# Optimization experiments

Measured on AMD Instinct MI355X. Metric: run time of the kernel, lower is better.

## Reference

```python
import jax, jax.numpy as jnp
import numpy as np

V, E, L, H, B, T = 32000, 1024, 6, 16, 4, 1024
HS = E // H
FF = 4 * E


def setup_inputs() -> dict:
    key = jax.random.key(0)
    ks = jax.random.split(key, 16)
    s = 0.02
    n = lambda k, shp: jax.random.normal(k, shp, jnp.float32) * s
    return {
        "tokens": jax.random.randint(ks[0], (B, T), 0, V),
        "tok_emb": n(ks[1], (V, E)),
        "pos_emb": n(ks[2], (T, E)),
        "Wq": n(ks[3], (L, E, E)),
        "Wk": n(ks[4], (L, E, E)),
        "Wv": n(ks[5], (L, E, E)),
        "Wo": n(ks[6], (L, E, E)),
        "ln1_g": jnp.ones((L, E), jnp.float32),
        "ln1_b": jnp.zeros((L, E), jnp.float32),
        "W1": n(ks[7], (L, E, FF)),
        "b1": jnp.zeros((L, FF), jnp.float32),
        "W2": n(ks[8], (L, FF, E)),
        "b2": jnp.zeros((L, E), jnp.float32),
        "ln2_g": jnp.ones((L, E), jnp.float32),
        "ln2_b": jnp.zeros((L, E), jnp.float32),
        "lmh_w": n(ks[9], (E, V)),
        "lmh_b": jnp.zeros((V,), jnp.float32),
    }


def _layernorm(x, g, b):
    m = jnp.mean(x, axis=-1, keepdims=True)
    v = jnp.var(x, axis=-1, keepdims=True)
    return (x - m) * jax.lax.rsqrt(v + 1e-5) * g + b


def _forward(tokens, tok_emb, pos_emb, Wq, Wk, Wv, Wo, ln1_g, ln1_b,
             W1, b1, W2, b2, ln2_g, ln2_b, lmh_w, lmh_b):
    Bb, Tt = tokens.shape
    x = tok_emb[tokens] + pos_emb[:Tt]  # [B,T,E]
    mask = jnp.tril(jnp.ones((Tt, Tt), bool))  # causal
    scale = jnp.float32(E) ** -0.5  # NOTE: original scales by emb_dim, not head_size

    def block(x, p):
        wq, wk, wv, wo, g1, be1, w1, bb1, w2, bb2, g2, be2 = p
        h = _layernorm(x, g1, be1)
        q = (h @ wq).reshape(Bb, Tt, H, HS)
        k = (h @ wk).reshape(Bb, Tt, H, HS)
        v = (h @ wv).reshape(Bb, Tt, H, HS)
        scores = jnp.einsum('bqhd,bkhd->bhqk', q, k) * scale
        scores = jnp.where(mask, scores, -jnp.inf)
        w = jax.nn.softmax(scores, axis=-1)
        attn = jnp.einsum('bhqk,bkhd->bqhd', w, v).reshape(Bb, Tt, E)
        x = x + attn @ wo
        h2 = _layernorm(x, g2, be2)
        x = x + jax.nn.relu(h2 @ w1 + bb1) @ w2 + bb2
        return x, None

    x, _ = jax.lax.scan(block, x, (Wq, Wk, Wv, Wo, ln1_g, ln1_b,
                                   W1, b1, W2, b2, ln2_g, ln2_b))
    logits = x @ lmh_w + lmh_b  # [B,T,V]
    return logits


def reference(tokens, tok_emb, pos_emb, Wq, Wk, Wv, Wo, ln1_g, ln1_b,
              W1, b1, W2, b2, ln2_g, ln2_b, lmh_w, lmh_b):
    return _forward(tokens, tok_emb, pos_emb, Wq, Wk, Wv, Wo, ln1_g, ln1_b,
                    W1, b1, W2, b2, ln2_g, ln2_b, lmh_w, lmh_b)
```

## Files before the change

kernel.cpp:

```cpp
#include <hip/hip_runtime.h>
#include <cstdint>
#include <cstddef>

typedef __bf16 bf16;
typedef __attribute__((ext_vector_type(8))) __bf16 bf16x8;
typedef __attribute__((ext_vector_type(4))) float f32x4;

constexpr int kV = 32000, kE = 1024, kL = 6, kH = 16, kB = 4, kT = 1024;
constexpr int kHS = 64, kFF = 4096;
constexpr int kM = kB * kT;
constexpr float kScale = 0.03125f;

typedef __attribute__((address_space(1))) void gv_t;
typedef __attribute__((address_space(3))) void lv_t;

__device__ inline void gload_lds16(const void* g, void* l) {
  __builtin_amdgcn_global_load_lds((gv_t*)g, (lv_t*)l, 16, 0, 0);
}

#define SB0() __builtin_amdgcn_sched_barrier(0)
#define LGK0() asm volatile("s_waitcnt lgkmcnt(0)" ::: "memory")

enum { EPI_BF16 = 0, EPI_BF16_BIAS_RELU = 1, EPI_F32 = 2, EPI_F32_RES = 3, EPI_F32_BIAS = 4 };

__device__ inline void xcd_swz(int& bx, int& by) {
  int gx = gridDim.x, gy = gridDim.y;
  int nxy = gx * gy;
  int orig = by * gx + bx;
  int q = nxy >> 3, r = nxy & 7, xcd = orig & 7, idx = orig >> 3;
  int logical = (xcd < r ? xcd * (q + 1) : r * (q + 1) + (xcd - r) * q) + idx;
  bx = logical / gy;
  by = logical % gy;
}

template <int EPI>
__global__ __launch_bounds__(512, 2) void gemm256_k(
    const bf16* __restrict__ Ag, const bf16* __restrict__ Bg, void* Cg,
    const float* __restrict__ bias, const float* __restrict__ resid,
    int K, long lda, long ldb, long ldc) {
  extern __shared__ bf16 lds[];
  constexpr int SL = 8192;
  bf16* As = lds;
  bf16* Bs = lds + 4 * SL;

  const int tid = threadIdx.x, lane = tid & 63, w = tid >> 6;
  int bx = blockIdx.x, by = blockIdx.y;
  xcd_swz(bx, by);
  const long tm = (long)by * 256, tn = (long)bx * 256;
  const int wr = w >> 2, wc = w & 3;
  const int lr = lane & 15, kg = lane >> 4;

  const int p0 = tid, p1 = 512 + tid;
  const int r0 = p0 >> 2, ls0 = (p0 & 3) ^ ((r0 >> 1) & 3);
  const int r1 = p1 >> 2, ls1 = (p1 & 3) ^ ((r1 >> 1) & 3);
  const bf16* a0 = Ag + (tm + r0) * lda + ls0 * 8;
  const bf16* a1 = Ag + (tm + r1) * lda + ls1 * 8;
  const bf16* b0 = Bg + (tn + r0) * ldb + ls0 * 8;
  const bf16* b1 = Bg + (tn + r1) * ldb + ls1 * 8;
  const int wb = w * 1024;

  auto stage = [&](int s) {
    const int slot = s & 3;
    const long k0 = (long)s * 32;
    char* Ab = (char*)As + slot * (SL * 2);
    char* Bb = (char*)Bs + slot * (SL * 2);
    gload_lds16(a0 + k0, Ab + wb);
    gload_lds16(a1 + k0, Ab + 8192 + wb);
    gload_lds16(b0 + k0, Bb + wb);
    gload_lds16(b1 + k0, Bb + 8192 + wb);
  };

  int aoff[8], boff[4];
#pragma unroll
  for (int mi = 0; mi < 8; mi++) {
    int ar = wr * 128 + mi * 16 + lr;
    aoff[mi] = ar * 64 + ((kg ^ ((ar >> 1) & 3)) << 4);
  }
#pragma unroll
  for (int ni = 0; ni < 4; ni++) {
    int br = wc * 64 + ni * 16 + lr;
    boff[ni] = br * 64 + ((kg ^ ((br >> 1) & 3)) << 4);
  }

  f32x4 acc[8][4] = {};
  stage(0);
  stage(1);
  stage(2);
  const int NS = K >> 5;
  for (int s = 0; s < NS; s++) {
    SB0();
    if (s <= NS - 3)
      asm volatile("s_waitcnt vmcnt(8)" ::: "memory");
    else if (s == NS - 2)
      asm volatile("s_waitcnt vmcnt(4)" ::: "memory");
    else
      asm volatile("s_waitcnt vmcnt(0)" ::: "memory");
    __builtin_amdgcn_s_barrier();
    SB0();
    if (s + 3 < NS) stage(s + 3);
    const char* Ab = (const char*)As + (s & 3) * (SL * 2);
    const char* Bb = (const char*)Bs + (s & 3) * (SL * 2);
    bf16x8 af[8], bfr[4];
#pragma unroll
    for (int mi = 0; mi < 8; mi++) af[mi] = *(const bf16x8*)(Ab + aoff[mi]);
#pragma unroll
    for (int ni = 0; ni < 4; ni++) bfr[ni] = *(const bf16x8*)(Bb + boff[ni]);
    __builtin_amdgcn_s_setprio(1);
#pragma unroll
    for (int mi = 0; mi < 8; mi++)
#pragma unroll
      for (int ni = 0; ni < 4; ni++)
        acc[mi][ni] =
            __builtin_amdgcn_mfma_f32_16x16x32_bf16(af[mi], bfr[ni], acc[mi][ni], 0, 0, 0);
    __builtin_amdgcn_s_setprio(0);
  }

#pragma unroll
  for (int mi = 0; mi < 8; mi++) {
#pragma unroll
    for (int ni = 0; ni < 4; ni++) {
      const long rr = tm + wr * 128 + mi * 16 + kg * 4;
      const long cc = tn + wc * 64 + ni * 16 + lr;
      float bi = 0.f;
      if constexpr (EPI == EPI_BF16_BIAS_RELU || EPI == EPI_F32_BIAS) bi = bias[cc];
      if constexpr (EPI == EPI_F32_RES) bi = bias ? bias[cc] : 0.f;
#pragma unroll
      for (int j = 0; j < 4; j++) {
        long off = (rr + j) * ldc + cc;
        float val = acc[mi][ni][j];
        if constexpr (EPI == EPI_BF16)
          ((bf16*)Cg)[off] = (bf16)val;
        else if constexpr (EPI == EPI_BF16_BIAS_RELU)
          ((bf16*)Cg)[off] = (bf16)fmaxf(val + bi, 0.f);
        else if constexpr (EPI == EPI_F32)
          ((float*)Cg)[off] = val;
        else if constexpr (EPI == EPI_F32_RES)
          ((float*)Cg)[off] = resid[off] + val + bi;
        else
          ((float*)Cg)[off] = val + bi;
      }
    }
  }
}

template <int EPI>
__global__ __launch_bounds__(256, 2) void ring128_k(
    const bf16* __restrict__ Ag, const bf16* __restrict__ Bg, void* Cg,
    const float* __restrict__ bias, const float* __restrict__ resid,
    int K, long lda, long ldb, long ldc) {
  extern __shared__ bf16 lds[];
  char* Lb = (char*)lds;
  const int tid = threadIdx.x, lane = tid & 63, w = tid >> 6;
  int bx = blockIdx.x, by = blockIdx.y;
  xcd_swz(bx, by);
  const long tm = (long)by * 128, tn = (long)bx * 128;
  const int wr = w >> 1, wc = w & 1;
  const int lr = lane & 15, kg = lane >> 4;

  const int r0 = tid >> 2, g0 = (tid & 3) ^ ((r0 >> 1) & 3);
  const int r1 = (256 + tid) >> 2, g1 = ((256 + tid) & 3) ^ ((r1 >> 1) & 3);
  const bf16* a0 = Ag + (tm + r0) * lda + g0 * 8;
  const bf16* a1 = Ag + (tm + r1) * lda + g1 * 8;
  const bf16* b0 = Bg + (tn + r0) * ldb + g0 * 8;
  const bf16* b1 = Bg + (tn + r1) * ldb + g1 * 8;
  const int wb = w * 1024;

  auto stage = [&](int s) {
    const int slot = s & 3;
    const long k0 = (long)s * 32;
    char* Ab = Lb + slot * 16384;
    char* Bb = Ab + 8192;
    gload_lds16(a0 + k0, Ab + wb);
    gload_lds16(a1 + k0, Ab + 4096 + wb);
    gload_lds16(b0 + k0, Bb + wb);
    gload_lds16(b1 + k0, Bb + 4096 + wb);
  };

  int aoff[4], boff[4];
#pragma unroll
  for (int mi = 0; mi < 4; mi++) {
    int ar = wr * 64 + mi * 16 + lr;
    aoff[mi] = ar * 64 + ((kg ^ ((ar >> 1) & 3)) << 4);
  }
#pragma unroll
  for (int ni = 0; ni < 4; ni++) {
    int br = wc * 64 + ni * 16 + lr;
    boff[ni] = br * 64 + ((kg ^ ((br >> 1) & 3)) << 4);
  }

  f32x4 acc[4][4] = {};
  stage(0);
  stage(1);
  stage(2);
  const int NS = K >> 5;
  for (int s = 0; s < NS; s++) {
    SB0();
    if (s <= NS - 3)
      asm volatile("s_waitcnt vmcnt(8)" ::: "memory");
    else if (s == NS - 2)
      asm volatile("s_waitcnt vmcnt(4)" ::: "memory");
    else
      asm volatile("s_waitcnt vmcnt(0)" ::: "memory");
    __builtin_amdgcn_s_barrier();
    SB0();
    if (s + 3 < NS) stage(s + 3);
    const char* Ab = Lb + (s & 3) * 16384;
    const char* Bb = Ab + 8192;
    bf16x8 af[4], bfr[4];
#pragma unroll
    for (int mi = 0; mi < 4; mi++) af[mi] = *(const bf16x8*)(Ab + aoff[mi]);
#pragma unroll
    for (int ni = 0; ni < 4; ni++) bfr[ni] = *(const bf16x8*)(Bb + boff[ni]);
    __builtin_amdgcn_s_setprio(1);
#pragma unroll
    for (int mi = 0; mi < 4; mi++)
#pragma unroll
      for (int ni = 0; ni < 4; ni++)
        acc[mi][ni] =
            __builtin_amdgcn_mfma_f32_16x16x32_bf16(af[mi], bfr[ni], acc[mi][ni], 0, 0, 0);
    __builtin_amdgcn_s_setprio(0);
  }

#pragma unroll
  for (int mi = 0; mi < 4; mi++) {
#pragma unroll
    for (int ni = 0; ni < 4; ni++) {
      const long rr = tm + wr * 64 + mi * 16 + kg * 4;
      const long cc = tn + wc * 64 + ni * 16 + lr;
      float bi = 0.f;
      if constexpr (EPI == EPI_BF16_BIAS_RELU || EPI == EPI_F32_BIAS) bi = bias[cc];
      if constexpr (EPI == EPI_F32_RES) bi = bias ? bias[cc] : 0.f;
#pragma unroll
      for (int j = 0; j < 4; j++) {
        long off = (rr + j) * ldc + cc;
        float val = acc[mi][ni][j];
        if constexpr (EPI == EPI_BF16)
          ((bf16*)Cg)[off] = (bf16)val;
        else if constexpr (EPI == EPI_BF16_BIAS_RELU)
          ((bf16*)Cg)[off] = (bf16)fmaxf(val + bi, 0.f);
        else if constexpr (EPI == EPI_F32)
          ((float*)Cg)[off] = val;
        else if constexpr (EPI == EPI_F32_RES)
          ((float*)Cg)[off] = resid[off] + val + bi;
        else
          ((float*)Cg)[off] = val + bi;
      }
    }
  }
}

__global__ __launch_bounds__(128) void fa_k(const bf16* __restrict__ qkv,
                                            const bf16* __restrict__ vtG,
                                            bf16* __restrict__ out) {
  extern __shared__ bf16 lds[];
  char* L = (char*)lds;
  const int tid = threadIdx.x, lane = tid & 63, wq = tid >> 6;
  const int lr = lane & 15, kg = lane >> 4;
  const int bh = blockIdx.x, z = blockIdx.y;
  const int b = bh >> 4, hh = bh & 15;
  const long bq = (long)b * kT;
  const int qt = z < 4 ? z : 11 - z;
  const int q0 = qt * 128;
  const bf16* qbase = qkv + (bq + q0) * 3072 + hh * 64;
  const bf16* vbase = vtG + (long)bh * 64 * kT;

#pragma unroll
  for (int i = 0; i < 8; i++) {
    int p = i * 128 + tid;
    int row = p >> 3, s = p & 7;
    gload_lds16(qbase + (long)row * 3072 + ((s ^ (row & 7)) * 8),
                L + (i * 128 + (tid & ~63)) * 16);
  }
  auto stageKV = [&](int buf, int t) {
    const bf16* kb = qkv + (bq + t * 64) * 3072 + 1024 + hh * 64;
    const bf16* vb = vbase + t * 64;
#pragma unroll
    for (int i = 0; i < 4; i++) {
      int p = i * 128 + tid;
      int key = p >> 3, s = p & 7;
      gload_lds16(kb + (long)key * 3072 + ((s ^ (key & 7)) * 8),
                  L + 16384 + buf * 8192 + (i * 128 + (tid & ~63)) * 16);
    }
#pragma unroll
    for (int i = 0; i < 4; i++) {
      int p = i * 128 + tid;
      int key = p >> 3, s = p & 7;
      gload_lds16(vb + (long)key * kT + s * 8,
                  L + 32768 + buf * 8192 + (i * 128 + (tid & ~63)) * 16);
    }
  };
  stageKV(0, 0);
  __syncthreads();

  bf16x8 qf[4][2];
#pragma unroll
  for (int qi = 0; qi < 4; qi++)
#pragma unroll
    for (int ks = 0; ks < 2; ks++) {
      int qr = wq * 64 + qi * 16 + lr;
      bf16x8 v = *(const bf16x8*)(L + qr * 128 + ((ks * 64 + kg * 16) ^ ((qr & 7) << 4)));
#pragma unroll
      for (int e = 0; e < 8; e++) v[e] = (bf16)((float)v[e] * kScale);
      qf[qi][ks] = v;
    }

  f32x4 O[4][4] = {};
  float lrun[4] = {0.f, 0.f, 0.f, 0.f};
  char* Pw = L + 49152 + wq * 9216;

  const int nt = 2 * qt + 2;
  int cur = 0;
  for (int t = 0; t < nt; t++) {
    if (t + 1 < nt) stageKV(cur ^ 1, t + 1);

    const char* Kb = L + 16384 + cur * 8192;
    f32x4 S[4][4] = {};
#pragma unroll
    for (int ks = 0; ks < 2; ks++) {
      bf16x8 kf[4];
#pragma unroll
      for (int ki = 0; ki < 4; ki++) {
        int key = ki * 16 + lr;
        kf[ki] = *(const bf16x8*)(Kb + key * 128 + ((ks * 64 + kg * 16) ^ ((key & 7) << 4)));
      }
#pragma unroll
      for (int ki = 0; ki < 4; ki++)
#pragma unroll
        for (int qi = 0; qi < 4; qi++)
          S[ki][qi] =
              __builtin_amdgcn_mfma_f32_16x16x32_bf16(kf[ki], qf[qi][ks], S[ki][qi], 0, 0, 0);
    }

    const int kvb = t * 64;
#pragma unroll
    for (int qi = 0; qi < 4; qi++) {
      const int q = q0 + wq * 64 + qi * 16 + lr;
      float ls = 0.f;
#pragma unroll
      for (int ki = 0; ki < 4; ki++) {
        union { bf16 h[4]; uint2 u; } pk;
#pragma unroll
        for (int j = 0; j < 4; j++) {
          int kv = kvb + ki * 16 + kg * 4 + j;
          float e = (kv <= q) ? __expf(S[ki][qi][j]) : 0.f;
          ls += e;
          pk.h[j] = (bf16)e;
        }
        *(uint2*)(Pw + (qi * 16 + lr) * 144 + (ki * 16 + kg * 4) * 2) = pk.u;
      }
      ls += __shfl_xor(ls, 16);
      ls += __shfl_xor(ls, 32);
      lrun[qi] += ls;
    }
    LGK0();
    SB0();

    const char* Vb = L + 32768 + cur * 8192;
#pragma unroll
    for (int ks = 0; ks < 2; ks++) {
      bf16x8 pf[4], vf[4];
#pragma unroll
      for (int qi = 0; qi < 4; qi++)
        pf[qi] = *(const bf16x8*)(Pw + (qi * 16 + lr) * 144 + ks * 64 + kg * 16);
#pragma unroll
      for (int di = 0; di < 4; di++) {
        int d = di * 16 + lr;
        vf[di] = *(const bf16x8*)(Vb + d * 128 + ((ks * 64 + kg * 16) ^ ((d & 7) << 4)));
      }
#pragma unroll
      for (int qi = 0; qi < 4; qi++)
#pragma unroll
        for (int di = 0; di < 4; di++)
          O[qi][di] =
              __builtin_amdgcn_mfma_f32_16x16x32_bf16(pf[qi], vf[di], O[qi][di], 0, 0, 0);
    }
    __syncthreads();
    cur ^= 1;
  }

#pragma unroll
  for (int qi = 0; qi < 4; qi++) {
#pragma unroll
    for (int j = 0; j < 4; j++) {
      float lv = __shfl(lrun[qi], kg * 4 + j);
      float inv = 1.f / lv;
      long grow = bq + q0 + wq * 64 + qi * 16 + kg * 4 + j;
#pragma unroll
      for (int di = 0; di < 4; di++)
        out[grow * kE + hh * 64 + di * 16 + lr] = (bf16)(O[qi][di][j] * inv);
    }
  }
}

__global__ void vtrans_k(const bf16* __restrict__ qkv, bf16* __restrict__ vt) {
  __shared__ bf16 tbuf[32][33];
  int z = blockIdx.z;
  int b = z >> 4, h = z & 15;
  int t0 = blockIdx.x * 32, s0 = blockIdx.y * 32;
  int tx = threadIdx.x, ty = threadIdx.y;
#pragma unroll
  for (int i = 0; i < 32; i += 8)
    tbuf[ty + i][tx] = qkv[((long)b * kT + t0 + ty + i) * 3072 + 2048 + h * 64 + s0 + tx];
  __syncthreads();
#pragma unroll
  for (int i = 0; i < 32; i += 8) {
    int d = s0 + ty + i;
    int tt = t0 + tx;
    int g = (tt >> 3) & 7, e = tt & 7;
    long idx = ((long)z * 64 + d) * kT + (tt & ~63) + ((g ^ (d & 7)) << 3) + e;
    vt[idx] = tbuf[tx][ty + i];
  }
}

__global__ void tcvt_k(const float* __restrict__ in, bf16* __restrict__ out, int K, int N,
                       long in_zs, long out_zs) {
  __shared__ float t[32][33];
  long z = blockIdx.z;
  in += z * in_zs;
  out += z * out_zs;
  int n0 = blockIdx.x * 32, k0 = blockIdx.y * 32;
  int tx = threadIdx.x, ty = threadIdx.y;
#pragma unroll
  for (int i = 0; i < 32; i += 8) t[ty + i][tx] = in[(long)(k0 + ty + i) * N + n0 + tx];
  __syncthreads();
#pragma unroll
  for (int i = 0; i < 32; i += 8)
    out[(long)(n0 + ty + i) * K + k0 + tx] = (bf16)t[tx][ty + i];
}

__global__ void embed_k(const int* __restrict__ toks, const float* __restrict__ te,
                        const float* __restrict__ pe, float* __restrict__ x) {
  int row = blockIdx.x, tid = threadIdx.x;
  int t = row & (kT - 1);
  long tok = toks[row];
  float4 a = ((const float4*)(te + tok * kE))[tid];
  float4 p = ((const float4*)(pe + (long)t * kE))[tid];
  float4 r{a.x + p.x, a.y + p.y, a.z + p.z, a.w + p.w};
  ((float4*)(x + (long)row * kE))[tid] = r;
}

__global__ void ln_k(const float* __restrict__ x, const float* __restrict__ g,
                     const float* __restrict__ b, bf16* __restrict__ h) {
  int row = blockIdx.x, tid = threadIdx.x, lane = tid & 63, w = tid >> 6;
  const float4 v = ((const float4*)(x + (long)row * kE))[tid];
  float s = v.x + v.y + v.z + v.w;
  float ss = v.x * v.x + v.y * v.y + v.z * v.z + v.w * v.w;
#pragma unroll
  for (int o = 32; o; o >>= 1) {
    s += __shfl_xor(s, o);
    ss += __shfl_xor(ss, o);
  }
  __shared__ float r1[4], r2[4];
  if (lane == 0) { r1[w] = s; r2[w] = ss; }
  __syncthreads();
  s = r1[0] + r1[1] + r1[2] + r1[3];
  ss = r2[0] + r2[1] + r2[2] + r2[3];
  float mean = s * (1.f / kE);
  float var = ss * (1.f / kE) - mean * mean;
  float rs = rsqrtf(var + 1e-5f);
  float4 gg = ((const float4*)g)[tid];
  float4 bb = ((const float4*)b)[tid];
  union { bf16 o[4]; uint2 u; } pk;
  pk.o[0] = (bf16)((v.x - mean) * rs * gg.x + bb.x);
  pk.o[1] = (bf16)((v.y - mean) * rs * gg.y + bb.y);
  pk.o[2] = (bf16)((v.z - mean) * rs * gg.z + bb.z);
  pk.o[3] = (bf16)((v.w - mean) * rs * gg.w + bb.w);
  ((uint2*)(h + (long)row * kE))[tid] = pk.u;
}

__global__ void cast_k(const float* __restrict__ x, bf16* __restrict__ o) {
  long i = (long)blockIdx.x * 256 + threadIdx.x;
  float4 v = ((const float4*)x)[i];
  union { bf16 b[4]; uint2 u; } pk;
  pk.b[0] = (bf16)v.x;
  pk.b[1] = (bf16)v.y;
  pk.b[2] = (bf16)v.z;
  pk.b[3] = (bf16)v.w;
  ((uint2*)o)[i] = pk.u;
}

extern "C" void kernel_launch(void* const* d_in, const int* in_sizes, int n_in,
                              void* d_out, int out_size, void* d_ws, size_t ws_size,
                              hipStream_t stream) {
  const int* toks = (const int*)d_in[0];
  const float* te = (const float*)d_in[1];
  const float* pe = (const float*)d_in[2];
  const float* Wq = (const float*)d_in[3];
  const float* Wk = (const float*)d_in[4];
  const float* Wv = (const float*)d_in[5];
  const float* Wo = (const float*)d_in[6];
  const float* g1 = (const float*)d_in[7];
  const float* be1 = (const float*)d_in[8];
  const float* W1 = (const float*)d_in[9];
  const float* bb1 = (const float*)d_in[10];
  const float* W2 = (const float*)d_in[11];
  const float* bb2 = (const float*)d_in[12];
  const float* g2 = (const float*)d_in[13];
  const float* be2 = (const float*)d_in[14];
  const float* lmw = (const float*)d_in[15];
  const float* lmb = (const float*)d_in[16];

  hipFuncSetAttribute(reinterpret_cast<const void*>(&gemm256_k<EPI_BF16>),
                      hipFuncAttributeMaxDynamicSharedMemorySize, 131072);
  hipFuncSetAttribute(reinterpret_cast<const void*>(&gemm256_k<EPI_BF16_BIAS_RELU>),
                      hipFuncAttributeMaxDynamicSharedMemorySize, 131072);
  hipFuncSetAttribute(reinterpret_cast<const void*>(&gemm256_k<EPI_F32_BIAS>),
                      hipFuncAttributeMaxDynamicSharedMemorySize, 131072);
  hipFuncSetAttribute(reinterpret_cast<const void*>(&ring128_k<EPI_F32_RES>),
                      hipFuncAttributeMaxDynamicSharedMemorySize, 65536);
  hipFuncSetAttribute(reinterpret_cast<const void*>(&fa_k),
                      hipFuncAttributeMaxDynamicSharedMemorySize, 67584);

  char* ws = (char*)d_ws;
  size_t off = 0;
  auto alloc = [&](size_t bytes) -> char* {
    char* p = ws + off;
    off += (bytes + 255) & ~(size_t)255;
    return p;
  };
  bf16* WqkvT = (bf16*)alloc((size_t)kL * 3 * kE * kE * 2);
  bf16* WoT = (bf16*)alloc((size_t)kL * kE * kE * 2);
  bf16* W1T = (bf16*)alloc((size_t)kL * kE * kFF * 2);
  bf16* W2T = (bf16*)alloc((size_t)kL * kE * kFF * 2);
  bf16* lmT = (bf16*)alloc((size_t)kV * kE * 2);
  float* x = (float*)alloc((size_t)kM * kE * 4);
  bf16* h = (bf16*)alloc((size_t)kM * kE * 2);
  bf16* qkv = (bf16*)alloc((size_t)kM * 3 * kE * 2);
  bf16* at = (bf16*)alloc((size_t)kM * kE * 2);
  bf16* vtG = (bf16*)alloc((size_t)kB * kH * 64 * kT * 2);

  bf16* mid = (bf16*)d_out;

  const long EE = (long)kE * kE;
  dim3 tb(32, 8);
  tcvt_k<<<dim3(kE / 32, kE / 32, kL), tb, 0, stream>>>(Wq, WqkvT, kE, kE, EE, 3 * EE);
  tcvt_k<<<dim3(kE / 32, kE / 32, kL), tb, 0, stream>>>(Wk, WqkvT + EE, kE, kE, EE, 3 * EE);
  tcvt_k<<<dim3(kE / 32, kE / 32, kL), tb, 0, stream>>>(Wv, WqkvT + 2 * EE, kE, kE, EE, 3 * EE);
  tcvt_k<<<dim3(kE / 32, kE / 32, kL), tb, 0, stream>>>(Wo, WoT, kE, kE, EE, EE);
  tcvt_k<<<dim3(kFF / 32, kE / 32, kL), tb, 0, stream>>>(W1, W1T, kE, kFF, 4 * EE, 4 * EE);
  tcvt_k<<<dim3(kE / 32, kFF / 32, kL), tb, 0, stream>>>(W2, W2T, kFF, kE, 4 * EE, 4 * EE);
  tcvt_k<<<dim3(kV / 32, kE / 32, 1), tb, 0, stream>>>(lmw, lmT, kE, kV, 0, 0);

  embed_k<<<kM, 256, 0, stream>>>(toks, te, pe, x);

  for (int l = 0; l < kL; l++) {
    ln_k<<<kM, 256, 0, stream>>>(x, g1 + l * kE, be1 + l * kE, h);
    gemm256_k<EPI_BF16><<<dim3(3 * kE / 256, kM / 256), 512, 131072, stream>>>(
        h, WqkvT + (size_t)l * 3 * EE, qkv, nullptr, nullptr, kE, kE, kE, 3 * kE);
    vtrans_k<<<dim3(kT / 32, kHS / 32, kB * kH), tb, 0, stream>>>(qkv, vtG);
    fa_k<<<dim3(kB * kH, 8), 128, 67584, stream>>>(qkv, vtG, at);
    ring128_k<EPI_F32_RES><<<dim3(kE / 128, kM / 128), 256, 65536, stream>>>(
        at, WoT + (size_t)l * EE, x, nullptr, x, kE, kE, kE, kE);
    ln_k<<<kM, 256, 0, stream>>>(x, g2 + l * kE, be2 + l * kE, h);
    gemm256_k<EPI_BF16_BIAS_RELU><<<dim3(kFF / 256, kM / 256), 512, 131072, stream>>>(
        h, W1T + (size_t)l * (size_t)kFF * kE, mid, bb1 + l * kFF, nullptr, kE, kE, kE, kFF);
    ring128_k<EPI_F32_RES><<<dim3(kE / 128, kM / 128), 256, 65536, stream>>>(
        mid, W2T + (size_t)l * (size_t)kE * kFF, x, bb2 + l * kE, x, kFF, kFF, kFF, kE);
  }
  cast_k<<<kM * kE / 1024, 256, 0, stream>>>(x, h);
  gemm256_k<EPI_F32_BIAS><<<dim3(kV / 256, kM / 256), 512, 131072, stream>>>(
      h, lmT, d_out, lmb, nullptr, kE, kE, kE, kV);
}
```

Baseline: 1.970 ms.

## Double-buffer GEMM LDS fragment reads and fold log2e into Q scale for exp2

The GEMM main loop is unrolled by two with ping-pong register fragments. LDS reads for the next k-step are issued before the MFMAs of the current step, so LDS latency is hidden behind matrix math and the vmcnt waits are adjusted to match. In attention, the Q pre-scale now includes log2(e), so the softmax exponent uses exp2f directly and skips a multiply. This raises VGPR pressure from the extra fragment buffers and makes the wait-count bookkeeping more fragile.

```diff
diff --git a/kernel.cpp b/kernel.cpp
--- a/kernel.cpp
+++ b/kernel.cpp
@@ -10,6 +10,7 @@
 constexpr int kHS = 64, kFF = 4096;
 constexpr int kM = kB * kT;
 constexpr float kScale = 0.03125f;
+constexpr float kQScale = 0.0451038961f;
 
 typedef __attribute__((address_space(1))) void gv_t;
 typedef __attribute__((address_space(3))) void lv_t;
@@ -189,35 +190,72 @@
   }
 
   f32x4 acc[4][4] = {};
+  bf16x8 afA[4], bfA[4], afB[4], bfB[4];
+
   stage(0);
   stage(1);
   stage(2);
+  asm volatile("s_waitcnt vmcnt(8)" ::: "memory");
+  __builtin_amdgcn_s_barrier();
+  SB0();
+  {
+    const char* Ab = Lb;
+    const char* Bb = Lb + 8192;
+#pragma unroll
+    for (int i = 0; i < 4; i++) afA[i] = *(const bf16x8*)(Ab + aoff[i]);
+#pragma unroll
+    for (int i = 0; i < 4; i++) bfA[i] = *(const bf16x8*)(Bb + boff[i]);
+  }
+
   const int NS = K >> 5;
-  for (int s = 0; s < NS; s++) {
+  for (int s = 0; s < NS; s += 2) {
     SB0();
-    if (s <= NS - 3)
-      asm volatile("s_waitcnt vmcnt(8)" ::: "memory");
-    else if (s == NS - 2)
+    if (s + 2 < NS)
       asm volatile("s_waitcnt vmcnt(4)" ::: "memory");
     else
       asm volatile("s_waitcnt vmcnt(0)" ::: "memory");
     __builtin_amdgcn_s_barrier();
     SB0();
     if (s + 3 < NS) stage(s + 3);
-    const char* Ab = Lb + (s & 3) * 16384;
-    const char* Bb = Ab + 8192;
-    bf16x8 af[4], bfr[4];
-#pragma unroll
-    for (int mi = 0; mi < 4; mi++) af[mi] = *(const bf16x8*)(Ab + aoff[mi]);
-#pragma unroll
-    for (int ni = 0; ni < 4; ni++) bfr[ni] = *(const bf16x8*)(Bb + boff[ni]);
+    {
+      const char* Ab = Lb + ((s + 1) & 3) * 16384;
+      const char* Bb = Ab + 8192;
+#pragma unroll
+      for (int i = 0; i < 4; i++) afB[i] = *(const bf16x8*)(Ab + aoff[i]);
+#pragma unroll
+      for (int i = 0; i < 4; i++) bfB[i] = *(const bf16x8*)(Bb + boff[i]);
+    }
     __builtin_amdgcn_s_setprio(1);
 #pragma unroll
     for (int mi = 0; mi < 4; mi++)
 #pragma unroll
       for (int ni = 0; ni < 4; ni++)
         acc[mi][ni] =
-            __builtin_amdgcn_mfma_f32_16x16x32_bf16(af[mi], bfr[ni], acc[mi][ni], 0, 0, 0);
+            __builtin_amdgcn_mfma_f32_16x16x32_bf16(afA[mi], bfA[ni], acc[mi][ni], 0, 0, 0);
+    __builtin_amdgcn_s_setprio(0);
+    if (s + 2 < NS) {
+      SB0();
+      if (s + 3 < NS)
+        asm volatile("s_waitcnt vmcnt(4)" ::: "memory");
+      else
+        asm volatile("s_waitcnt vmcnt(0)" ::: "memory");
+      __builtin_amdgcn_s_barrier();
+      SB0();
+      if (s + 4 < NS) stage(s + 4);
+      const char* Ab = Lb + ((s + 2) & 3) * 16384;
+      const char* Bb = Ab + 8192;
+#pragma unroll
+      for (int i = 0; i < 4; i++) afA[i] = *(const bf16x8*)(Ab + aoff[i]);
+#pragma unroll
+      for (int i = 0; i < 4; i++) bfA[i] = *(const bf16x8*)(Bb + boff[i]);
+    }
+    __builtin_amdgcn_s_setprio(1);
+#pragma unroll
+    for (int mi = 0; mi < 4; mi++)
+#pragma unroll
+      for (int ni = 0; ni < 4; ni++)
+        acc[mi][ni] =
+            __builtin_amdgcn_mfma_f32_16x16x32_bf16(afB[mi], bfB[ni], acc[mi][ni], 0, 0, 0);
     __builtin_amdgcn_s_setprio(0);
   }
 
@@ -300,7 +338,7 @@
       int qr = wq * 64 + qi * 16 + lr;
       bf16x8 v = *(const bf16x8*)(L + qr * 128 + ((ks * 64 + kg * 16) ^ ((qr & 7) << 4)));
 #pragma unroll
-      for (int e = 0; e < 8; e++) v[e] = (bf16)((float)v[e] * kScale);
+      for (int e = 0; e < 8; e++) v[e] = (bf16)((float)v[e] * kQScale);
       qf[qi][ks] = v;
     }
 
@@ -342,7 +380,7 @@
 #pragma unroll
         for (int j = 0; j < 4; j++) {
           int kv = kvb + ki * 16 + kg * 4 + j;
-          float e = (kv <= q) ? __expf(S[ki][qi][j]) : 0.f;
+          float e = (kv <= q) ? exp2f(S[ki][qi][j]) : 0.f;
           ls += e;
           pk.h[j] = (bf16)e;
         }
```

Result: slower. 2.053 ms (+4.2%).
